# Optimization experiments

Hardware: AMD Instinct MI355X
Metric: run time of the kernel (lower is better)

## Reference

```python
import jax, jax.numpy as jnp
import numpy as np

N_NODES = 50000


def _gcn_norm(edge_index, edge_weight, num_nodes):
    """Add self-loops (weight 1) and compute symmetric GCN normalization.
    Returns (src, dst, norm) over the augmented edge set."""
    src = jnp.concatenate([edge_index[0], jnp.arange(num_nodes, dtype=edge_index.dtype)])
    dst = jnp.concatenate([edge_index[1], jnp.arange(num_nodes, dtype=edge_index.dtype)])
    w = jnp.concatenate([edge_weight, jnp.ones((num_nodes,), dtype=edge_weight.dtype)])
    deg = jax.ops.segment_sum(w, dst, num_segments=num_nodes)  # [N]
    deg_inv_sqrt = jnp.where(deg > 0, jax.lax.rsqrt(jnp.where(deg > 0, deg, 1.0)), 0.0)
    norm = deg_inv_sqrt[src] * w * deg_inv_sqrt[dst]  # [E+N]
    return src, dst, norm


def _gcn_conv(x, W, b, src, dst, norm, num_nodes):
    h = x @ W                                   # [N, out] linear first (PyG order)
    msg = h[src] * norm[:, None]                # [E+N, out] gather + scale
    out = jax.ops.segment_sum(msg, dst, num_segments=num_nodes)  # scatter-add
    return out + b


def setup_inputs() -> dict:
    key = jax.random.key(0)
    ks = jax.random.split(key, 9)
    N, E = N_NODES, 800000
    x = jax.random.normal(ks[0], (N, 256), dtype=jnp.float32)
    edge_index = jax.random.randint(ks[1], (2, E), 0, N, dtype=jnp.int64)
    edge_attr = jax.random.uniform(ks[2], (E,), dtype=jnp.float32)
    W1 = jax.random.normal(ks[3], (256, 128), dtype=jnp.float32) * (1.0 / np.sqrt(256))
    b1 = jnp.zeros((128,), dtype=jnp.float32)
    W2 = jax.random.normal(ks[4], (128, 128), dtype=jnp.float32) * (1.0 / np.sqrt(128))
    b2 = jnp.zeros((128,), dtype=jnp.float32)
    W3 = jax.random.normal(ks[5], (128, 128), dtype=jnp.float32) * (1.0 / np.sqrt(128))
    b3 = jnp.zeros((128,), dtype=jnp.float32)
    return {"x": x, "edge_index": edge_index, "edge_attr": edge_attr,
            "W1": W1, "b1": b1, "W2": W2, "b2": b2, "W3": W3, "b3": b3}


def reference(x, edge_index, edge_attr, W1, b1, W2, b2, W3, b3):
    N = x.shape[0]
    src, dst, norm = _gcn_norm(edge_index, edge_attr, N)
    x1 = jax.nn.relu(_gcn_conv(x, W1, b1, src, dst, norm, N))
    x2 = jax.nn.relu(_gcn_conv(x1, W2, b2, src, dst, norm, N))
    return jax.nn.relu(_gcn_conv(x2, W3, b3, src, dst, norm, N))
```

## Files before the change

kernel.cpp:

```cpp
#include <hip/hip_runtime.h>
#include <math.h>

#define F_OUT 128
#define MAXDEG 64

typedef __attribute__((ext_vector_type(8))) short short8v;
typedef __attribute__((ext_vector_type(4))) float f32x4;
typedef unsigned long long ull;

__device__ inline ushort f2bf(float x) {
    uint u = __float_as_uint(x);
    uint r = (u + 0x7FFFu + ((u >> 16) & 1u)) >> 16;
    return (ushort)r;
}
__device__ inline float bf2f(ushort h) { return __uint_as_float((uint)h << 16); }
__device__ inline uint pack2(ushort a, ushort b) { return (uint)a | ((uint)b << 16); }


__global__ __launch_bounds__(128) void prep_kernel(const float* __restrict__ W1,
                                                   ushort* W1th, ushort* W1tl,
                                                   ull* slot, int n) {
    int b = blockIdx.x;
    if (b < 256) {
        int idx = b * 128 + threadIdx.x;
        int k = idx >> 7, c = idx & 127;
        float x = W1[idx];
        ushort h = f2bf(x);
        ushort l = f2bf(x - bf2f(h));
        W1th[(size_t)c * 256 + k] = h;
        W1tl[(size_t)c * 256 + k] = l;
    } else {
        int i = (b - 256) * 128 + threadIdx.x;
        if (i < n) slot[i] = 0ull;
    }
}


__device__ __forceinline__ void fill_edge(const int* __restrict__ src,
                                          const int* __restrict__ dst,
                                          const float* __restrict__ w,
                                          ull* slot, int2* es, int e) {
    int s = src[e], d = dst[e];
    float wv = w[e];
    ull inc = (1ull << 40) | (ull)(uint)(wv * 8388608.0f + 0.5f);
    ull old = atomicAdd(&slot[d], inc);
    uint pos = (uint)(old >> 40);
    if (pos < MAXDEG) es[(size_t)d * MAXDEG + pos] = make_int2(s, __float_as_int(wv));
}

__global__ void dis_kernel(const ull* __restrict__ slot, float* dis, int n) {
    int i = blockIdx.x * blockDim.x + threadIdx.x;
    if (i < n) {
        float sumw = (float)((double)(slot[i] & ((1ull << 40) - 1)) * (1.0 / 8388608.0));
        dis[i] = rsqrtf(1.0f + sumw);
    }
}

__global__ void coef_kernel(int2* es, const ull* __restrict__ slot,
                            const float* __restrict__ dis, int n) {
    int i = blockIdx.x * blockDim.x + threadIdx.x;
    if (i < n * MAXDEG) {
        int d = i >> 6;
        int pos = i & (MAXDEG - 1);
        int cnt = (int)(slot[d] >> 40);
        if (pos < cnt) {
            int2 e = es[i];
            es[i].y = __float_as_int(dis[e.x] * __int_as_float(e.y));
        }
    }
}


template <int K>
__device__ __forceinline__ void gemm_body(ushort* sAh, ushort* sAl,
                                          ushort* sBh, ushort* sBl,
                                          const float* __restrict__ in,
                                          const ushort* __restrict__ Wth,
                                          const ushort* __restrict__ Wtl,
                                          ushort* __restrict__ hbf, int n, int bb) {
    const int t = threadIdx.x;
    const int lane = t & 63;
    const int wv = t >> 6;
    const int block_row = bb * 64;

    const int arow = t >> 1;
    const int ahalf = t & 1;
    const int bcol = t;

    const int l15 = lane & 15;
    const int koct = lane >> 4;

    f32x4 acc[4][4];
    #pragma unroll
    for (int r = 0; r < 4; ++r)
        #pragma unroll
        for (int c = 0; c < 4; ++c) acc[r][c] = (f32x4){0.f, 0.f, 0.f, 0.f};

    const int grow_a = block_row + arow;
    const bool arow_ok = grow_a < n;

    for (int kt = 0; kt < K / 32; ++kt) {
        const int k0 = kt * 32;

        {
            float v[16];
            if (arow_ok) {
                const float4* p = reinterpret_cast<const float4*>(
                    &in[(size_t)grow_a * K + k0 + ahalf * 16]);
                float4 f0 = p[0], f1 = p[1], f2 = p[2], f3 = p[3];
                v[0]=f0.x; v[1]=f0.y; v[2]=f0.z; v[3]=f0.w;
                v[4]=f1.x; v[5]=f1.y; v[6]=f1.z; v[7]=f1.w;
                v[8]=f2.x; v[9]=f2.y; v[10]=f2.z; v[11]=f2.w;
                v[12]=f3.x; v[13]=f3.y; v[14]=f3.z; v[15]=f3.w;
            } else {
                #pragma unroll
                for (int i = 0; i < 16; ++i) v[i] = 0.f;
            }
            ushort hh[16], ll[16];
            #pragma unroll
            for (int i = 0; i < 16; ++i) {
                hh[i] = f2bf(v[i]);
                ll[i] = f2bf(v[i] - bf2f(hh[i]));
            }
            const int c0 = 2 * ahalf, c1 = 2 * ahalf + 1;
            *reinterpret_cast<uint4*>(&sAh[(c0 * 64 + arow) * 8]) =
                make_uint4(pack2(hh[0],hh[1]), pack2(hh[2],hh[3]), pack2(hh[4],hh[5]), pack2(hh[6],hh[7]));
            *reinterpret_cast<uint4*>(&sAh[(c1 * 64 + arow) * 8]) =
                make_uint4(pack2(hh[8],hh[9]), pack2(hh[10],hh[11]), pack2(hh[12],hh[13]), pack2(hh[14],hh[15]));
            *reinterpret_cast<uint4*>(&sAl[(c0 * 64 + arow) * 8]) =
                make_uint4(pack2(ll[0],ll[1]), pack2(ll[2],ll[3]), pack2(ll[4],ll[5]), pack2(ll[6],ll[7]));
            *reinterpret_cast<uint4*>(&sAl[(c1 * 64 + arow) * 8]) =
                make_uint4(pack2(ll[8],ll[9]), pack2(ll[10],ll[11]), pack2(ll[12],ll[13]), pack2(ll[14],ll[15]));
        }
        {
            const uint4* ph = reinterpret_cast<const uint4*>(&Wth[(size_t)bcol * K + k0]);
            const uint4* pl = reinterpret_cast<const uint4*>(&Wtl[(size_t)bcol * K + k0]);
            #pragma unroll
            for (int j = 0; j < 4; ++j)
                *reinterpret_cast<uint4*>(&sBh[(j * 128 + bcol) * 8]) = ph[j];
            #pragma unroll
            for (int j = 0; j < 4; ++j)
                *reinterpret_cast<uint4*>(&sBl[(j * 128 + bcol) * 8]) = pl[j];
        }
        __syncthreads();

        short8v a_h[4], a_l[4], b_h[4], b_l[4];
        #pragma unroll
        for (int r = 0; r < 4; ++r) {
            a_h[r] = *reinterpret_cast<const short8v*>(&sAh[(koct * 64 + r * 16 + l15) * 8]);
            a_l[r] = *reinterpret_cast<const short8v*>(&sAl[(koct * 64 + r * 16 + l15) * 8]);
        }
        #pragma unroll
        for (int c = 0; c < 4; ++c) {
            b_h[c] = *reinterpret_cast<const short8v*>(&sBh[(koct * 128 + wv * 64 + c * 16 + l15) * 8]);
            b_l[c] = *reinterpret_cast<const short8v*>(&sBl[(koct * 128 + wv * 64 + c * 16 + l15) * 8]);
        }

        #pragma unroll
        for (int r = 0; r < 4; ++r)
            #pragma unroll
            for (int c = 0; c < 4; ++c) {
                acc[r][c] = __builtin_amdgcn_mfma_f32_16x16x32_bf16(a_h[r], b_h[c], acc[r][c], 0, 0, 0);
                acc[r][c] = __builtin_amdgcn_mfma_f32_16x16x32_bf16(a_h[r], b_l[c], acc[r][c], 0, 0, 0);
                acc[r][c] = __builtin_amdgcn_mfma_f32_16x16x32_bf16(a_l[r], b_h[c], acc[r][c], 0, 0, 0);
            }
        __syncthreads();
    }

    #pragma unroll
    for (int r = 0; r < 4; ++r) {
        #pragma unroll
        for (int c = 0; c < 4; ++c) {
            int gcol = wv * 64 + c * 16 + l15;
            #pragma unroll
            for (int j = 0; j < 4; ++j) {
                int grow = block_row + r * 16 + koct * 4 + j;
                if (grow < n) hbf[(size_t)grow * F_OUT + gcol] = f2bf(acc[r][c][j]);
            }
        }
    }
}


__global__ __launch_bounds__(128) void mega1_kernel(
        const float* __restrict__ x,
        const ushort* __restrict__ W1th, const ushort* __restrict__ W1tl,
        ushort* __restrict__ hbf,
        const int* __restrict__ src, const int* __restrict__ dst,
        const float* __restrict__ w, ull* slot, int2* es,
        const float* __restrict__ W2, ushort* W2th, ushort* W2tl,
        const float* __restrict__ W3, ushort* W3th, ushort* W3tl,
        int n, int E, int GB, int FB) {
    __shared__ ushort sAh[64 * 32], sAl[64 * 32];
    __shared__ ushort sBh[128 * 32], sBl[128 * 32];

    int b = blockIdx.x;
    if (b < GB) {
        gemm_body<256>(sAh, sAl, sBh, sBl, x, W1th, W1tl, hbf, n, b);
    } else if (b < GB + FB) {
        int e = (b - GB) * 128 + threadIdx.x;
        if (e < E) fill_edge(src, dst, w, slot, es, e);
    } else {
        int wb = b - GB - FB;
        const float* W = (wb < 128) ? W2 : W3;
        ushort* Th = (wb < 128) ? W2th : W3th;
        ushort* Tl = (wb < 128) ? W2tl : W3tl;
        int idx = (wb & 127) * 128 + threadIdx.x;
        int k = idx >> 7, c = idx & 127;
        float v = W[idx];
        ushort h = f2bf(v);
        ushort l = f2bf(v - bf2f(h));
        Th[(size_t)c * 128 + k] = h;
        Tl[(size_t)c * 128 + k] = l;
    }
}


template <int K>
__global__ __launch_bounds__(128) void gemm_mfma(const float* __restrict__ in,
                                                 const ushort* __restrict__ Wth,
                                                 const ushort* __restrict__ Wtl,
                                                 ushort* __restrict__ hbf, int n) {
    __shared__ ushort sAh[64 * 32], sAl[64 * 32];
    __shared__ ushort sBh[128 * 32], sBl[128 * 32];
    gemm_body<K>(sAh, sAl, sBh, sBl, in, Wth, Wtl, hbf, n, blockIdx.x);
}


__device__ __forceinline__ void gacc(uint u, float c, float& ax, float& ay) {
    ax += c * __uint_as_float(u << 16);
    ay += c * __uint_as_float(u & 0xFFFF0000u);
}

__global__ __launch_bounds__(256) void gather_kernel(const ushort* __restrict__ hbf,
                                                     const int2* __restrict__ es,
                                                     const ull* __restrict__ slot,
                                                     const float* __restrict__ dis,
                                                     const float* __restrict__ bias,
                                                     float* __restrict__ out, int n) {
    int wave = threadIdx.x >> 6;
    int lane = threadIdx.x & 63;
    int node = blockIdx.x * 4 + wave;
    if (node >= n) return;

    int f = lane * 2;
    float dd = dis[node];
    int cnt = (int)(slot[node] >> 40);
    if (cnt > MAXDEG) cnt = MAXDEG;

    uint hv = *reinterpret_cast<const uint*>(&hbf[(size_t)node * F_OUT + f]);
    float accx = dd * __uint_as_float(hv << 16);
    float accy = dd * __uint_as_float(hv & 0xFFFF0000u);

    const int2* ep = es + (size_t)node * MAXDEG;
    int i = 0;
    for (; i + 7 < cnt; i += 8) {
        int4 p01 = *reinterpret_cast<const int4*>(&ep[i]);
        int4 p23 = *reinterpret_cast<const int4*>(&ep[i + 2]);
        int4 p45 = *reinterpret_cast<const int4*>(&ep[i + 4]);
        int4 p67 = *reinterpret_cast<const int4*>(&ep[i + 6]);
        uint u0 = *reinterpret_cast<const uint*>(&hbf[(size_t)p01.x * F_OUT + f]);
        uint u1 = *reinterpret_cast<const uint*>(&hbf[(size_t)p01.z * F_OUT + f]);
        uint u2 = *reinterpret_cast<const uint*>(&hbf[(size_t)p23.x * F_OUT + f]);
        uint u3 = *reinterpret_cast<const uint*>(&hbf[(size_t)p23.z * F_OUT + f]);
        uint u4 = *reinterpret_cast<const uint*>(&hbf[(size_t)p45.x * F_OUT + f]);
        uint u5 = *reinterpret_cast<const uint*>(&hbf[(size_t)p45.z * F_OUT + f]);
        uint u6 = *reinterpret_cast<const uint*>(&hbf[(size_t)p67.x * F_OUT + f]);
        uint u7 = *reinterpret_cast<const uint*>(&hbf[(size_t)p67.z * F_OUT + f]);
        gacc(u0, __int_as_float(p01.y), accx, accy);
        gacc(u1, __int_as_float(p01.w), accx, accy);
        gacc(u2, __int_as_float(p23.y), accx, accy);
        gacc(u3, __int_as_float(p23.w), accx, accy);
        gacc(u4, __int_as_float(p45.y), accx, accy);
        gacc(u5, __int_as_float(p45.w), accx, accy);
        gacc(u6, __int_as_float(p67.y), accx, accy);
        gacc(u7, __int_as_float(p67.w), accx, accy);
    }
    for (; i + 1 < cnt; i += 2) {
        int4 p01 = *reinterpret_cast<const int4*>(&ep[i]);
        uint u0 = *reinterpret_cast<const uint*>(&hbf[(size_t)p01.x * F_OUT + f]);
        uint u1 = *reinterpret_cast<const uint*>(&hbf[(size_t)p01.z * F_OUT + f]);
        gacc(u0, __int_as_float(p01.y), accx, accy);
        gacc(u1, __int_as_float(p01.w), accx, accy);
    }
    if (i < cnt) {
        int2 e0 = ep[i];
        uint u0 = *reinterpret_cast<const uint*>(&hbf[(size_t)e0.x * F_OUT + f]);
        gacc(u0, __int_as_float(e0.y), accx, accy);
    }

    float2 r;
    r.x = fmaxf(bias[f]     + dd * accx, 0.f);
    r.y = fmaxf(bias[f + 1] + dd * accy, 0.f);
    *reinterpret_cast<float2*>(&out[(size_t)node * F_OUT + f]) = r;
}


extern "C" void kernel_launch(void* const* d_in, const int* in_sizes, int n_in,
                              void* d_out, int out_size, void* d_ws, size_t ws_size,
                              hipStream_t stream) {
    const float* x  = (const float*)d_in[0];
    const int*   ei = (const int*)  d_in[1];
    const float* ew = (const float*)d_in[2];
    const float* W1 = (const float*)d_in[3];
    const float* b1 = (const float*)d_in[4];
    const float* W2 = (const float*)d_in[5];
    const float* b2 = (const float*)d_in[6];
    const float* W3 = (const float*)d_in[7];
    const float* b3 = (const float*)d_in[8];
    float* out = (float*)d_out;

    const int E = in_sizes[2];
    const int n = in_sizes[0] / 256;
    const int* src = ei;
    const int* dst = ei + E;

    char* ws = (char*)d_ws;
    ull*   slot  = (ull*)ws;
    int2*  es    = (int2*)(slot + n);
    float* act   = (float*)(es + (size_t)n * MAXDEG);
    float* dis   = act + (size_t)n * F_OUT;
    ushort* hbf  = (ushort*)(dis + n);
    ushort* W1th = hbf + (size_t)n * F_OUT;
    ushort* W1tl = W1th + 128 * 256;
    ushort* W2th = W1tl + 128 * 256;
    ushort* W2tl = W2th + 128 * 128;
    ushort* W3th = W2tl + 128 * 128;
    ushort* W3tl = W3th + 128 * 128;

    const int GB = (n + 63) / 64;
    const int FB = (E + 127) / 128;
    const int prep_grid = 256 + (n + 127) / 128;

    prep_kernel<<<prep_grid, 128, 0, stream>>>(W1, W1th, W1tl, slot, n);

    mega1_kernel<<<GB + FB + 256, 128, 0, stream>>>(
        x, W1th, W1tl, hbf, src, dst, ew, slot, es,
        W2, W2th, W2tl, W3, W3th, W3tl, n, E, GB, FB);

    dis_kernel<<<(n + 255) / 256, 256, 0, stream>>>(slot, dis, n);
    coef_kernel<<<(n * MAXDEG + 255) / 256, 256, 0, stream>>>(es, slot, dis, n);

    const int gather_grid = (n + 3) / 4;

    gather_kernel<<<gather_grid, 256, 0, stream>>>(hbf, es, slot, dis, b1, act, n);

    gemm_mfma<128><<<GB, 128, 0, stream>>>(act, W2th, W2tl, hbf, n);
    gather_kernel<<<gather_grid, 256, 0, stream>>>(hbf, es, slot, dis, b2, act, n);

    gemm_mfma<128><<<GB, 128, 0, stream>>>(act, W3th, W3tl, hbf, n);
    gather_kernel<<<gather_grid, 256, 0, stream>>>(hbf, es, slot, dis, b3, out, n);
}
```

Baseline: 227.9 us.

## Presplit gather outputs to bf16 hi/lo, fold dis into consumers, batch edge fill

The gather kernel now writes its activations directly as bf16 high/low halves, and a new gemm_presplit kernel loads those halves instead of reading fp32 and splitting them itself. The separate dis kernel is removed: the coefficient and gather kernels recompute rsqrt of the degree from the slot word inline. Each edge-fill block now handles 8 edges per thread, cutting the number of fill blocks. The aim is to drop one launch, shrink the activation traffic between layers, and avoid repeating the split work; in exchange there are redundant rsqrt/double conversions and an extra slot read per edge in the coefficient kernel.

```diff
diff --git a/kernel.cpp b/kernel.cpp
--- a/kernel.cpp
+++ b/kernel.cpp
@@ -15,6 +15,10 @@
 }
 __device__ inline float bf2f(ushort h) { return __uint_as_float((uint)h << 16); }
 __device__ inline uint pack2(ushort a, ushort b) { return (uint)a | ((uint)b << 16); }
+
+__device__ inline float slot_sumw(ull s) {
+    return (float)((double)(s & ((1ull << 40) - 1)) * (1.0 / 8388608.0));
+}
 
 
 __global__ __launch_bounds__(128) void prep_kernel(const float* __restrict__ W1,
@@ -48,16 +52,7 @@
     if (pos < MAXDEG) es[(size_t)d * MAXDEG + pos] = make_int2(s, __float_as_int(wv));
 }
 
-__global__ void dis_kernel(const ull* __restrict__ slot, float* dis, int n) {
-    int i = blockIdx.x * blockDim.x + threadIdx.x;
-    if (i < n) {
-        float sumw = (float)((double)(slot[i] & ((1ull << 40) - 1)) * (1.0 / 8388608.0));
-        dis[i] = rsqrtf(1.0f + sumw);
-    }
-}
-
-__global__ void coef_kernel(int2* es, const ull* __restrict__ slot,
-                            const float* __restrict__ dis, int n) {
+__global__ void coef_kernel(int2* es, const ull* __restrict__ slot, int n) {
     int i = blockIdx.x * blockDim.x + threadIdx.x;
     if (i < n * MAXDEG) {
         int d = i >> 6;
@@ -65,7 +60,8 @@
         int cnt = (int)(slot[d] >> 40);
         if (pos < cnt) {
             int2 e = es[i];
-            es[i].y = __float_as_int(dis[e.x] * __int_as_float(e.y));
+            float dsrc = rsqrtf(1.0f + slot_sumw(slot[e.x]));
+            es[i].y = __float_as_int(dsrc * __int_as_float(e.y));
         }
     }
 }
@@ -155,7 +151,103 @@
             b_h[c] = *reinterpret_cast<const short8v*>(&sBh[(koct * 128 + wv * 64 + c * 16 + l15) * 8]);
             b_l[c] = *reinterpret_cast<const short8v*>(&sBl[(koct * 128 + wv * 64 + c * 16 + l15) * 8]);
         }
-
+        #pragma unroll
+        for (int r = 0; r < 4; ++r)
+            #pragma unroll
+            for (int c = 0; c < 4; ++c) {
+                acc[r][c] = __builtin_amdgcn_mfma_f32_16x16x32_bf16(a_h[r], b_h[c], acc[r][c], 0, 0, 0);
+                acc[r][c] = __builtin_amdgcn_mfma_f32_16x16x32_bf16(a_h[r], b_l[c], acc[r][c], 0, 0, 0);
+                acc[r][c] = __builtin_amdgcn_mfma_f32_16x16x32_bf16(a_l[r], b_h[c], acc[r][c], 0, 0, 0);
+            }
+        __syncthreads();
+    }
+
+    #pragma unroll
+    for (int r = 0; r < 4; ++r) {
+        #pragma unroll
+        for (int c = 0; c < 4; ++c) {
+            int gcol = wv * 64 + c * 16 + l15;
+            #pragma unroll
+            for (int j = 0; j < 4; ++j) {
+                int grow = block_row + r * 16 + koct * 4 + j;
+                if (grow < n) hbf[(size_t)grow * F_OUT + gcol] = f2bf(acc[r][c][j]);
+            }
+        }
+    }
+}
+
+
+template <int K>
+__global__ __launch_bounds__(128) void gemm_presplit(const ushort* __restrict__ ahp,
+                                                     const ushort* __restrict__ alp,
+                                                     const ushort* __restrict__ Wth,
+                                                     const ushort* __restrict__ Wtl,
+                                                     ushort* __restrict__ hbf, int n) {
+    __shared__ ushort sAh[64 * 32], sAl[64 * 32];
+    __shared__ ushort sBh[128 * 32], sBl[128 * 32];
+
+    const int t = threadIdx.x;
+    const int lane = t & 63;
+    const int wv = t >> 6;
+    const int block_row = blockIdx.x * 64;
+
+    const int arow = t >> 1;
+    const int ahalf = t & 1;
+    const int bcol = t;
+
+    const int l15 = lane & 15;
+    const int koct = lane >> 4;
+
+    f32x4 acc[4][4];
+    #pragma unroll
+    for (int r = 0; r < 4; ++r)
+        #pragma unroll
+        for (int c = 0; c < 4; ++c) acc[r][c] = (f32x4){0.f, 0.f, 0.f, 0.f};
+
+    const int grow_a = block_row + arow;
+    const bool arow_ok = grow_a < n;
+    const uint4 zero4 = make_uint4(0u, 0u, 0u, 0u);
+
+    for (int kt = 0; kt < K / 32; ++kt) {
+        const int k0 = kt * 32;
+        const int c0 = 2 * ahalf, c1 = 2 * ahalf + 1;
+
+        if (arow_ok) {
+            const uint4* ph = reinterpret_cast<const uint4*>(&ahp[(size_t)grow_a * K + k0 + ahalf * 16]);
+            const uint4* pl = reinterpret_cast<const uint4*>(&alp[(size_t)grow_a * K + k0 + ahalf * 16]);
+            *reinterpret_cast<uint4*>(&sAh[(c0 * 64 + arow) * 8]) = ph[0];
+            *reinterpret_cast<uint4*>(&sAh[(c1 * 64 + arow) * 8]) = ph[1];
+            *reinterpret_cast<uint4*>(&sAl[(c0 * 64 + arow) * 8]) = pl[0];
+            *reinterpret_cast<uint4*>(&sAl[(c1 * 64 + arow) * 8]) = pl[1];
+        } else {
+            *reinterpret_cast<uint4*>(&sAh[(c0 * 64 + arow) * 8]) = zero4;
+            *reinterpret_cast<uint4*>(&sAh[(c1 * 64 + arow) * 8]) = zero4;
+            *reinterpret_cast<uint4*>(&sAl[(c0 * 64 + arow) * 8]) = zero4;
+            *reinterpret_cast<uint4*>(&sAl[(c1 * 64 + arow) * 8]) = zero4;
+        }
+        {
+            const uint4* ph = reinterpret_cast<const uint4*>(&Wth[(size_t)bcol * K + k0]);
+            const uint4* pl = reinterpret_cast<const uint4*>(&Wtl[(size_t)bcol * K + k0]);
+            #pragma unroll
+            for (int j = 0; j < 4; ++j)
+                *reinterpret_cast<uint4*>(&sBh[(j * 128 + bcol) * 8]) = ph[j];
+            #pragma unroll
+            for (int j = 0; j < 4; ++j)
+                *reinterpret_cast<uint4*>(&sBl[(j * 128 + bcol) * 8]) = pl[j];
+        }
+        __syncthreads();
+
+        short8v a_h[4], a_l[4], b_h[4], b_l[4];
+        #pragma unroll
+        for (int r = 0; r < 4; ++r) {
+            a_h[r] = *reinterpret_cast<const short8v*>(&sAh[(koct * 64 + r * 16 + l15) * 8]);
+            a_l[r] = *reinterpret_cast<const short8v*>(&sAl[(koct * 64 + r * 16 + l15) * 8]);
+        }
+        #pragma unroll
+        for (int c = 0; c < 4; ++c) {
+            b_h[c] = *reinterpret_cast<const short8v*>(&sBh[(koct * 128 + wv * 64 + c * 16 + l15) * 8]);
+            b_l[c] = *reinterpret_cast<const short8v*>(&sBl[(koct * 128 + wv * 64 + c * 16 + l15) * 8]);
+        }
         #pragma unroll
         for (int r = 0; r < 4; ++r)
             #pragma unroll
@@ -198,8 +290,12 @@
     if (b < GB) {
         gemm_body<256>(sAh, sAl, sBh, sBl, x, W1th, W1tl, hbf, n, b);
     } else if (b < GB + FB) {
-        int e = (b - GB) * 128 + threadIdx.x;
-        if (e < E) fill_edge(src, dst, w, slot, es, e);
+        int ebase = (b - GB) * 1024 + threadIdx.x;
+        #pragma unroll
+        for (int q = 0; q < 8; ++q) {
+            int e = ebase + q * 128;
+            if (e < E) fill_edge(src, dst, w, slot, es, e);
+        }
     } else {
         int wb = b - GB - FB;
         const float* W = (wb < 128) ? W2 : W3;
@@ -216,37 +312,29 @@
 }
 
 
-template <int K>
-__global__ __launch_bounds__(128) void gemm_mfma(const float* __restrict__ in,
-                                                 const ushort* __restrict__ Wth,
-                                                 const ushort* __restrict__ Wtl,
-                                                 ushort* __restrict__ hbf, int n) {
-    __shared__ ushort sAh[64 * 32], sAl[64 * 32];
-    __shared__ ushort sBh[128 * 32], sBl[128 * 32];
-    gemm_body<K>(sAh, sAl, sBh, sBl, in, Wth, Wtl, hbf, n, blockIdx.x);
-}
-
-
 __device__ __forceinline__ void gacc(uint u, float c, float& ax, float& ay) {
     ax += c * __uint_as_float(u << 16);
     ay += c * __uint_as_float(u & 0xFFFF0000u);
 }
 
+template <bool SPLIT_OUT>
 __global__ __launch_bounds__(256) void gather_kernel(const ushort* __restrict__ hbf,
                                                      const int2* __restrict__ es,
                                                      const ull* __restrict__ slot,
-                                                     const float* __restrict__ dis,
                                                      const float* __restrict__ bias,
-                                                     float* __restrict__ out, int n) {
+                                                     ushort* __restrict__ oah,
+                                                     ushort* __restrict__ oal,
+                                                     float* __restrict__ outf, int n) {
     int wave = threadIdx.x >> 6;
     int lane = threadIdx.x & 63;
     int node = blockIdx.x * 4 + wave;
     if (node >= n) return;
 
     int f = lane * 2;
-    float dd = dis[node];
-    int cnt = (int)(slot[node] >> 40);
+    ull sl = slot[node];
+    int cnt = (int)(sl >> 40);
     if (cnt > MAXDEG) cnt = MAXDEG;
+    float dd = rsqrtf(1.0f + slot_sumw(sl));
 
     uint hv = *reinterpret_cast<const uint*>(&hbf[(size_t)node * F_OUT + f]);
     float accx = dd * __uint_as_float(hv << 16);
@@ -289,10 +377,17 @@
         gacc(u0, __int_as_float(e0.y), accx, accy);
     }
 
-    float2 r;
-    r.x = fmaxf(bias[f]     + dd * accx, 0.f);
-    r.y = fmaxf(bias[f + 1] + dd * accy, 0.f);
-    *reinterpret_cast<float2*>(&out[(size_t)node * F_OUT + f]) = r;
+    float rx = fmaxf(bias[f]     + dd * accx, 0.f);
+    float ry = fmaxf(bias[f + 1] + dd * accy, 0.f);
+
+    if (SPLIT_OUT) {
+        ushort hx = f2bf(rx), hy = f2bf(ry);
+        ushort lx = f2bf(rx - bf2f(hx)), ly = f2bf(ry - bf2f(hy));
+        *reinterpret_cast<uint*>(&oah[(size_t)node * F_OUT + f]) = pack2(hx, hy);
+        *reinterpret_cast<uint*>(&oal[(size_t)node * F_OUT + f]) = pack2(lx, ly);
+    } else {
+        *reinterpret_cast<float2*>(&outf[(size_t)node * F_OUT + f]) = make_float2(rx, ry);
+    }
 }
 
 
@@ -318,10 +413,10 @@
     char* ws = (char*)d_ws;
     ull*   slot  = (ull*)ws;
     int2*  es    = (int2*)(slot + n);
-    float* act   = (float*)(es + (size_t)n * MAXDEG);
-    float* dis   = act + (size_t)n * F_OUT;
-    ushort* hbf  = (ushort*)(dis + n);
-    ushort* W1th = hbf + (size_t)n * F_OUT;
+    ushort* hbf  = (ushort*)(es + (size_t)n * MAXDEG);
+    ushort* aah  = hbf + (size_t)n * F_OUT;
+    ushort* aal  = aah + (size_t)n * F_OUT;
+    ushort* W1th = aal + (size_t)n * F_OUT;
     ushort* W1tl = W1th + 128 * 256;
     ushort* W2th = W1tl + 128 * 256;
     ushort* W2tl = W2th + 128 * 128;
@@ -329,7 +424,7 @@
     ushort* W3tl = W3th + 128 * 128;
 
     const int GB = (n + 63) / 64;
-    const int FB = (E + 127) / 128;
+    const int FB = (E + 1023) / 1024;
     const int prep_grid = 256 + (n + 127) / 128;
 
     prep_kernel<<<prep_grid, 128, 0, stream>>>(W1, W1th, W1tl, slot, n);
@@ -338,16 +433,15 @@
         x, W1th, W1tl, hbf, src, dst, ew, slot, es,
         W2, W2th, W2tl, W3, W3th, W3tl, n, E, GB, FB);
 
-    dis_kernel<<<(n + 255) / 256, 256, 0, stream>>>(slot, dis, n);
-    coef_kernel<<<(n * MAXDEG + 255) / 256, 256, 0, stream>>>(es, slot, dis, n);
+    coef_kernel<<<(n * MAXDEG + 255) / 256, 256, 0, stream>>>(es, slot, n);
 
     const int gather_grid = (n + 3) / 4;
 
-    gather_kernel<<<gather_grid, 256, 0, stream>>>(hbf, es, slot, dis, b1, act, n);
-
-    gemm_mfma<128><<<GB, 128, 0, stream>>>(act, W2th, W2tl, hbf, n);
-    gather_kernel<<<gather_grid, 256, 0, stream>>>(hbf, es, slot, dis, b2, act, n);
-
-    gemm_mfma<128><<<GB, 128, 0, stream>>>(act, W3th, W3tl, hbf, n);
-    gather_kernel<<<gather_grid, 256, 0, stream>>>(hbf, es, slot, dis, b3, out, n);
-}
+    gather_kernel<true><<<gather_grid, 256, 0, stream>>>(hbf, es, slot, b1, aah, aal, nullptr, n);
+
+    gemm_presplit<128><<<GB, 128, 0, stream>>>(aah, aal, W2th, W2tl, hbf, n);
+    gather_kernel<true><<<gather_grid, 256, 0, stream>>>(hbf, es, slot, b2, aah, aal, nullptr, n);
+
+    gemm_presplit<128><<<GB, 128, 0, stream>>>(aah, aal, W3th, W3tl, hbf, n);
+    gather_kernel<false><<<gather_grid, 256, 0, stream>>>(hbf, es, slot, b3, nullptr, nullptr, out, n);
+}
```

New measurement: 208.2 us. -8.6%, faster.
